# Optimization experiments

Hardware: AMD Instinct MI355X
Metric: run time of the kernel (lower is better)

## Reference

```python
import jax, jax.numpy as jnp
import numpy as np

B = 8192
D = 1024
NUM_CLASSES = 100


def setup_inputs() -> dict:
    key = jax.random.key(0)
    kx, ky = jax.random.split(key)
    x = jax.random.normal(kx, (B, D), dtype=jnp.float32)
    y = jax.random.randint(ky, (B,), 0, NUM_CLASSES, dtype=jnp.int64)
    return {"x": x, "y": y, "T": 1}


def reference(x, y, T):
    b = x.shape[0]
    # Pairwise Euclidean distances via Gram matrix (same math as
    # torch.norm(x[:,None]-x, dim=2) without the b*b*d intermediate).
    xn = jnp.sum(x * x, axis=1)                      # [b]
    d2 = xn[None, :] + xn[:, None] - 2.0 * (x @ x.T)  # [b, b]
    d2 = jnp.maximum(d2, 0.0)
    eye = jnp.eye(b, dtype=bool)
    # Diagonal is masked to -inf below; plug 1.0 to keep sqrt well-defined.
    dist = jnp.sqrt(jnp.where(eye, 1.0, d2))
    e_dist = -dist * T
    neg_inf = jnp.float32(-jnp.inf)
    # Denominator: all pairs except self.
    den_dist = jnp.where(eye, neg_inf, e_dist)
    # Numerator: same-label pairs except self.
    same = (y[None, :] == y[:, None]) & ~eye
    num_dist = jnp.where(same, e_dist, neg_inf)
    num = jax.nn.logsumexp(num_dist, axis=1)         # [b]
    den = jax.nn.logsumexp(den_dist, axis=1)         # [b]
    # Original fixup: anchors with no positives (num == -inf) contribute 0 to num;
    # den is re-indexed by isinf(num) AFTER num was zeroed, so den is unchanged.
    num = jnp.where(jnp.isinf(num), 0.0, num)
    return -jnp.mean(num - den)
```

## Files before the change

### kernel.cpp

```cpp
#include <hip/hip_runtime.h>
#include <hip/hip_bf16.h>
#include <stdint.h>

#define BN 8192
#define DK 1024
#define NTILES 2080

typedef __attribute__((ext_vector_type(4))) float f32x4;

__device__ __forceinline__ unsigned int f2e4m3(float f) {
  const unsigned int u = __float_as_uint(f);
  const unsigned int sign = (u >> 24) & 0x80u;
  float a = fabsf(f);
  if (a >= 448.f) return sign | 0x7Eu;
  if (a < 0.015625f) {
    int m = (int)rintf(a * 512.f);
    return sign | (unsigned int)m;
  }
  unsigned int x = __float_as_uint(a);
  x += 0x7FFFFu + ((x >> 20) & 1u);
  const unsigned int e = (x >> 23) - 127u + 7u;
  const unsigned int m = (x >> 20) & 7u;
  return sign | (e << 4) | m;
}

__global__ __launch_bounds__(256) void snn_prep(const float* __restrict__ x,
                                                unsigned char* __restrict__ xb,
                                                float* __restrict__ xn,
                                                float* __restrict__ den,
                                                float* __restrict__ num) {
  const int row = blockIdx.x * 4 + (threadIdx.x >> 6);
  const int lane = threadIdx.x & 63;
  const float4* src = (const float4*)(x + (size_t)row * DK) + lane * 4;
  float s = 0.f;
  unsigned int pk[4];
#pragma unroll
  for (int i = 0; i < 4; ++i) {
    float4 v = src[i];
    s = fmaf(v.x, v.x, s); s = fmaf(v.y, v.y, s);
    s = fmaf(v.z, v.z, s); s = fmaf(v.w, v.w, s);
    pk[i] = f2e4m3(v.x) | (f2e4m3(v.y) << 8) | (f2e4m3(v.z) << 16) |
            (f2e4m3(v.w) << 24);
  }
  const int g = lane >> 3;
  const int c = lane & 7;
  const int r = row & 15;
  unsigned long long lo = (unsigned long long)pk[0] | ((unsigned long long)pk[1] << 32);
  unsigned long long hi = (unsigned long long)pk[2] | ((unsigned long long)pk[3] << 32);
  unsigned char* rowp = xb + (size_t)row * DK + g * 128;
  *(unsigned long long*)(rowp + (((2 * c) ^ r) << 3)) = lo;
  *(unsigned long long*)(rowp + (((2 * c + 1) ^ r) << 3)) = hi;
#pragma unroll
  for (int m = 32; m >= 1; m >>= 1) s += __shfl_xor(s, m);
  if (lane == 0) {
    xn[row] = s;
    den[row] = 0.f;
    num[row] = 0.f;
  }
}

__global__ __launch_bounds__(256, 4) void snn_main(
    const unsigned char* __restrict__ xb, const float* __restrict__ xn,
    const int* __restrict__ y, const unsigned int* __restrict__ Tp,
    float* __restrict__ den, float* __restrict__ num) {
  __shared__ __align__(16) unsigned char As[128 * 128];
  __shared__ __align__(16) unsigned char Bs[128 * 128];
  __shared__ float xnA[128], xnB[128];
  __shared__ int yA[128], yB[128];

  const int t = threadIdx.x;
  const int lane = t & 63;
  const int w = t >> 6;
  const int wr = w >> 1, wc = w & 1;
  const int l15 = lane & 15;
  const int lg = lane >> 4;

  const int bid = blockIdx.x;
  const int ts = (bid & 7) * (NTILES / 8) + (bid >> 3);
  int I = (int)(64.5f - sqrtf(64.5f * 64.5f - 2.0f * (float)ts));
  while (I > 0 && (64 * I - (I * (I - 1)) / 2) > ts) --I;
  while ((64 * (I + 1) - ((I + 1) * I) / 2) <= ts) ++I;
  const int J = I + (ts - (64 * I - (I * (I - 1)) / 2));
  const int r0 = I * 128, c0 = J * 128;
  const bool diag = (I == J);

  const unsigned int tu = *Tp;
  const float tf = (tu & 0x7f800000u) ? __uint_as_float(tu) : (float)(int)tu;

  if (t < 128) {
    xnA[t] = xn[r0 + t]; yA[t] = y[r0 + t];
    xnB[t] = xn[c0 + t]; yB[t] = y[c0 + t];
  }

  f32x4 acc[4][4];
#pragma unroll
  for (int mi = 0; mi < 4; ++mi)
#pragma unroll
    for (int ni = 0; ni < 4; ++ni) acc[mi][ni] = (f32x4){0.f, 0.f, 0.f, 0.f};

  for (int kt = 0; kt < DK; kt += 128) {
#pragma unroll
    for (int i = 0; i < 4; ++i) {
      const int linear = i * 256 + t;
      const int row = linear >> 3;
      const int cg = linear & 7;
      const unsigned char* sa = xb + (size_t)(r0 + row) * DK + kt + cg * 16;
      const unsigned char* sb = xb + (size_t)(c0 + row) * DK + kt + cg * 16;
      __builtin_amdgcn_global_load_lds(
          (const __attribute__((address_space(1))) void*)sa,
          (__attribute__((address_space(3))) void*)(As + linear * 16), 16, 0, 0);
      __builtin_amdgcn_global_load_lds(
          (const __attribute__((address_space(1))) void*)sb,
          (__attribute__((address_space(3))) void*)(Bs + linear * 16), 16, 0, 0);
    }
    __syncthreads();
#pragma unroll
    for (int kk = 0; kk < 4; ++kk) {
      const int so = 4 * kk + lg;
      const int off = ((so ^ l15) << 3);
      long aL[4], bL[4];
#pragma unroll
      for (int mi = 0; mi < 4; ++mi) {
        const int row = wr * 64 + mi * 16 + l15;
        aL[mi] = *(const long*)(As + row * 128 + off);
      }
#pragma unroll
      for (int ni = 0; ni < 4; ++ni) {
        const int row = wc * 64 + ni * 16 + l15;
        bL[ni] = *(const long*)(Bs + row * 128 + off);
      }
#pragma unroll
      for (int mi = 0; mi < 4; ++mi)
#pragma unroll
        for (int ni = 0; ni < 4; ++ni)
          acc[mi][ni] = __builtin_amdgcn_mfma_f32_16x16x32_fp8_fp8(
              aL[mi], bL[ni], acc[mi][ni], 0, 0, 0);
    }
    __syncthreads();
  }

  float cxn[4]; int cy[4];
#pragma unroll
  for (int ni = 0; ni < 4; ++ni) {
    const int c_l = wc * 64 + ni * 16 + l15;
    cxn[ni] = xnB[c_l]; cy[ni] = yB[c_l];
  }
#pragma unroll
  for (int mi = 0; mi < 4; ++mi) {
#pragma unroll
    for (int rg = 0; rg < 4; ++rg) {
      const int row_l = wr * 64 + mi * 16 + lg * 4 + rg;
      const int rG = r0 + row_l;
      const float rxn = xnA[row_l];
      const int ry = yA[row_l];
      float u = 0.f, av = 0.f;
#pragma unroll
      for (int ni = 0; ni < 4; ++ni) {
        const int cG = c0 + wc * 64 + ni * 16 + l15;
        const float a = acc[mi][ni][rg];
        const float d2 = fmaxf(rxn + cxn[ni] - 2.0f * a, 0.f);
        const float p = (rG == cG) ? 0.f : __expf(-sqrtf(d2) * tf);
        const float v = (ry == cy[ni]) ? -p : p;
        acc[mi][ni][rg] = v;
        u += v; av += fabsf(v);
      }
#pragma unroll
      for (int mm = 8; mm >= 1; mm >>= 1) {
        u += __shfl_xor(u, mm); av += __shfl_xor(av, mm);
      }
      if (l15 == 0) {
        atomicAdd(&den[rG], av);
        atomicAdd(&num[rG], 0.5f * (av - u));
      }
    }
  }
  if (!diag) {
#pragma unroll
    for (int ni = 0; ni < 4; ++ni) {
      float u = 0.f, av = 0.f;
#pragma unroll
      for (int mi = 0; mi < 4; ++mi)
#pragma unroll
        for (int rg = 0; rg < 4; ++rg) {
          const float v = acc[mi][ni][rg];
          u += v; av += fabsf(v);
        }
      u += __shfl_xor(u, 16); av += __shfl_xor(av, 16);
      u += __shfl_xor(u, 32); av += __shfl_xor(av, 32);
      if (lg == 0) {
        const int cG = c0 + wc * 64 + ni * 16 + l15;
        atomicAdd(&den[cG], av);
        atomicAdd(&num[cG], 0.5f * (av - u));
      }
    }
  }
}

__global__ __launch_bounds__(256) void snn_final(const float* __restrict__ den,
                                                 const float* __restrict__ num,
                                                 float* __restrict__ out) {
  __shared__ float red[256];
  const int t = threadIdx.x;
  float local = 0.f;
  for (int r = t; r < BN; r += 256) {
    const float sd = den[r], sn = num[r];
    const float d = logf(sd);
    const float n = (sn > 0.f) ? logf(sn) : 0.f;
    local += d - n;
  }
  red[t] = local;
  __syncthreads();
  for (int s = 128; s >= 1; s >>= 1) {
    if (t < s) red[t] += red[t + s];
    __syncthreads();
  }
  if (t == 0) out[0] = red[0] * (1.0f / (float)BN);
}

extern "C" void kernel_launch(void* const* d_in, const int* in_sizes, int n_in,
                              void* d_out, int out_size, void* d_ws, size_t ws_size,
                              hipStream_t stream) {
  const float* x = (const float*)d_in[0];
  const int* y = (const int*)d_in[1];
  const unsigned int* Tp = (const unsigned int*)d_in[2];
  float* out = (float*)d_out;

  char* ws = (char*)d_ws;
  unsigned char* xb = (unsigned char*)ws;
  float* xn = (float*)(ws + (size_t)BN * DK);
  float* den = xn + BN;
  float* num = den + BN;

  snn_prep<<<dim3(BN / 4), dim3(256), 0, stream>>>(x, xb, xn, den, num);
  snn_main<<<dim3(NTILES), dim3(256), 0, stream>>>(xb, xn, y, Tp, den, num);
  snn_final<<<dim3(1), dim3(256), 0, stream>>>(den, num, out);
}
```

Baseline: 123.9 us.

## Double-buffer K-tiles in LDS, widen fragment loads, parallelize final reduction

The main GEMM loop now stages 64-byte K slices into two LDS buffers and prefetches the next slice while MFMAs run on the current one, so a barrier no longer sits between every load and its compute. The prep kernel switches to a matching 16-byte XOR swizzle, which lets each lane fetch a 128-bit fragment that feeds two MFMAs. The final log-sum reduction spreads over 32 blocks with an atomic add into an output zeroed by prep, replacing the single-block loop. The cost is twice as many barrier iterations and LDS-buffer pairs, plus a floating-point atomic whose summation order is not fixed.

```diff
diff --git a/kernel.cpp b/kernel.cpp
--- a/kernel.cpp
+++ b/kernel.cpp
@@ -7,6 +7,7 @@
 #define NTILES 2080
 
 typedef __attribute__((ext_vector_type(4))) float f32x4;
+typedef __attribute__((ext_vector_type(2))) long long2v;
 
 __device__ __forceinline__ unsigned int f2e4m3(float f) {
   const unsigned int u = __float_as_uint(f);
@@ -28,7 +29,8 @@
                                                 unsigned char* __restrict__ xb,
                                                 float* __restrict__ xn,
                                                 float* __restrict__ den,
-                                                float* __restrict__ num) {
+                                                float* __restrict__ num,
+                                                float* __restrict__ out) {
   const int row = blockIdx.x * 4 + (threadIdx.x >> 6);
   const int lane = threadIdx.x & 63;
   const float4* src = (const float4*)(x + (size_t)row * DK) + lane * 4;
@@ -42,20 +44,17 @@
     pk[i] = f2e4m3(v.x) | (f2e4m3(v.y) << 8) | (f2e4m3(v.z) << 16) |
             (f2e4m3(v.w) << 24);
   }
-  const int g = lane >> 3;
-  const int c = lane & 7;
-  const int r = row & 15;
-  unsigned long long lo = (unsigned long long)pk[0] | ((unsigned long long)pk[1] << 32);
-  unsigned long long hi = (unsigned long long)pk[2] | ((unsigned long long)pk[3] << 32);
-  unsigned char* rowp = xb + (size_t)row * DK + g * 128;
-  *(unsigned long long*)(rowp + (((2 * c) ^ r) << 3)) = lo;
-  *(unsigned long long*)(rowp + (((2 * c + 1) ^ r) << 3)) = hi;
+  const int g = lane >> 2;
+  const int c = lane & 3;
+  uint4 o; o.x = pk[0]; o.y = pk[1]; o.z = pk[2]; o.w = pk[3];
+  *(uint4*)(xb + (size_t)row * DK + g * 64 + ((c ^ (row & 3)) << 4)) = o;
 #pragma unroll
   for (int m = 32; m >= 1; m >>= 1) s += __shfl_xor(s, m);
   if (lane == 0) {
     xn[row] = s;
     den[row] = 0.f;
     num[row] = 0.f;
+    if (row == 0) out[0] = 0.f;
   }
 }
 
@@ -63,8 +62,8 @@
     const unsigned char* __restrict__ xb, const float* __restrict__ xn,
     const int* __restrict__ y, const unsigned int* __restrict__ Tp,
     float* __restrict__ den, float* __restrict__ num) {
-  __shared__ __align__(16) unsigned char As[128 * 128];
-  __shared__ __align__(16) unsigned char Bs[128 * 128];
+  __shared__ __align__(16) unsigned char As[2][128 * 64];
+  __shared__ __align__(16) unsigned char Bs[2][128 * 64];
   __shared__ float xnA[128], xnB[128];
   __shared__ int yA[128], yB[128];
 
@@ -92,50 +91,56 @@
     xnB[t] = xn[c0 + t]; yB[t] = y[c0 + t];
   }
 
-  f32x4 acc[4][4];
-#pragma unroll
-  for (int mi = 0; mi < 4; ++mi)
-#pragma unroll
-    for (int ni = 0; ni < 4; ++ni) acc[mi][ni] = (f32x4){0.f, 0.f, 0.f, 0.f};
-
-  for (int kt = 0; kt < DK; kt += 128) {
-#pragma unroll
-    for (int i = 0; i < 4; ++i) {
+  auto ISSUE = [&](int buf, int kt) {
+#pragma unroll
+    for (int i = 0; i < 2; ++i) {
       const int linear = i * 256 + t;
-      const int row = linear >> 3;
-      const int cg = linear & 7;
+      const int row = linear >> 2;
+      const int cg = linear & 3;
       const unsigned char* sa = xb + (size_t)(r0 + row) * DK + kt + cg * 16;
       const unsigned char* sb = xb + (size_t)(c0 + row) * DK + kt + cg * 16;
       __builtin_amdgcn_global_load_lds(
           (const __attribute__((address_space(1))) void*)sa,
-          (__attribute__((address_space(3))) void*)(As + linear * 16), 16, 0, 0);
+          (__attribute__((address_space(3))) void*)(As[buf] + linear * 16), 16, 0, 0);
       __builtin_amdgcn_global_load_lds(
           (const __attribute__((address_space(1))) void*)sb,
-          (__attribute__((address_space(3))) void*)(Bs + linear * 16), 16, 0, 0);
-    }
-    __syncthreads();
-#pragma unroll
-    for (int kk = 0; kk < 4; ++kk) {
-      const int so = 4 * kk + lg;
-      const int off = ((so ^ l15) << 3);
-      long aL[4], bL[4];
-#pragma unroll
-      for (int mi = 0; mi < 4; ++mi) {
-        const int row = wr * 64 + mi * 16 + l15;
-        aL[mi] = *(const long*)(As + row * 128 + off);
-      }
-#pragma unroll
-      for (int ni = 0; ni < 4; ++ni) {
-        const int row = wc * 64 + ni * 16 + l15;
-        bL[ni] = *(const long*)(Bs + row * 128 + off);
-      }
+          (__attribute__((address_space(3))) void*)(Bs[buf] + linear * 16), 16, 0, 0);
+    }
+  };
+
+  f32x4 acc[4][4];
+#pragma unroll
+  for (int mi = 0; mi < 4; ++mi)
+#pragma unroll
+    for (int ni = 0; ni < 4; ++ni) acc[mi][ni] = (f32x4){0.f, 0.f, 0.f, 0.f};
+
+  const int fro = (lg ^ (l15 & 3)) << 4;
+
+  ISSUE(0, 0);
+  __syncthreads();
+
+  for (int T = 0; T < 16; ++T) {
+    const int buf = T & 1;
+    if (T < 15) ISSUE(buf ^ 1, (T + 1) * 64);
+    long2v aF[4], bF[4];
+#pragma unroll
+    for (int mi = 0; mi < 4; ++mi) {
+      const int row = wr * 64 + mi * 16 + l15;
+      aF[mi] = *(const long2v*)(As[buf] + row * 64 + fro);
+    }
+#pragma unroll
+    for (int ni = 0; ni < 4; ++ni) {
+      const int row = wc * 64 + ni * 16 + l15;
+      bF[ni] = *(const long2v*)(Bs[buf] + row * 64 + fro);
+    }
+#pragma unroll
+    for (int kk = 0; kk < 2; ++kk)
 #pragma unroll
       for (int mi = 0; mi < 4; ++mi)
 #pragma unroll
         for (int ni = 0; ni < 4; ++ni)
           acc[mi][ni] = __builtin_amdgcn_mfma_f32_16x16x32_fp8_fp8(
-              aL[mi], bL[ni], acc[mi][ni], 0, 0, 0);
-    }
+              aF[mi][kk], bF[ni][kk], acc[mi][ni], 0, 0, 0);
     __syncthreads();
   }
 
@@ -201,20 +206,17 @@
                                                  float* __restrict__ out) {
   __shared__ float red[256];
   const int t = threadIdx.x;
-  float local = 0.f;
-  for (int r = t; r < BN; r += 256) {
-    const float sd = den[r], sn = num[r];
-    const float d = logf(sd);
-    const float n = (sn > 0.f) ? logf(sn) : 0.f;
-    local += d - n;
-  }
-  red[t] = local;
+  const int r = blockIdx.x * 256 + t;
+  const float sd = den[r], sn = num[r];
+  const float d = logf(sd);
+  const float n = (sn > 0.f) ? logf(sn) : 0.f;
+  red[t] = d - n;
   __syncthreads();
   for (int s = 128; s >= 1; s >>= 1) {
     if (t < s) red[t] += red[t + s];
     __syncthreads();
   }
-  if (t == 0) out[0] = red[0] * (1.0f / (float)BN);
+  if (t == 0) atomicAdd(out, red[0] * (1.0f / (float)BN));
 }
 
 extern "C" void kernel_launch(void* const* d_in, const int* in_sizes, int n_in,
@@ -231,7 +233,7 @@
   float* den = xn + BN;
   float* num = den + BN;
 
-  snn_prep<<<dim3(BN / 4), dim3(256), 0, stream>>>(x, xb, xn, den, num);
+  snn_prep<<<dim3(BN / 4), dim3(256), 0, stream>>>(x, xb, xn, den, num, out);
   snn_main<<<dim3(NTILES), dim3(256), 0, stream>>>(xb, xn, y, Tp, den, num);
-  snn_final<<<dim3(1), dim3(256), 0, stream>>>(den, num, out);
-}
+  snn_final<<<dim3(32), dim3(256), 0, stream>>>(den, num, out);
+}
```

Result: no change. 124.9 us (+0.8%).
